# Kernel optimization log

Measured on AMD Instinct MI355X. Metric: run time of the kernel, lower is better.

The kernel has to match this reference:

```python
import jax, jax.numpy as jnp
import numpy as np

DIM = 2048
N_HEADS = 16
Q_LORA = 1536
KV_LORA = 512
NOPE = 128
ROPE = 64
V_DIM = 128
QK_HEAD = NOPE + ROPE
SEQ = 4096
THETA = 10000.0
EPS = 1e-6
SCALE = QK_HEAD ** -0.5  # max_seq_len==4096 not >4096, so no mscale adjustment


def rms_norm(x, w):
    return x * jax.lax.rsqrt(jnp.mean(x * x, axis=-1, keepdims=True) + EPS) * w


def rope_cos_sin(seqlen):
    inv_freq = 1.0 / THETA ** (jnp.arange(0, ROPE, 2, dtype=jnp.float32) / ROPE)  # [ROPE/2]
    t = jnp.arange(seqlen, dtype=jnp.float32)
    freqs = jnp.outer(t, inv_freq)  # [S, ROPE/2]
    return jnp.cos(freqs), jnp.sin(freqs)


def apply_rope(x, cos, sin):
    # x: (b, s, h, ROPE); pairs (x0, x1) rotated as complex mult, interleaved layout
    b, s, h, d = x.shape
    xr = x.reshape(b, s, h, d // 2, 2)
    x0, x1 = xr[..., 0], xr[..., 1]
    c = cos[None, :, None, :]
    sn = sin[None, :, None, :]
    out = jnp.stack([x0 * c - x1 * sn, x0 * sn + x1 * c], axis=-1)
    return out.reshape(b, s, h, d)


def setup_inputs() -> dict:
    key = jax.random.key(0)
    ks = jax.random.split(key, 8)
    s = lambda fan_in: 1.0 / np.sqrt(fan_in)
    return {
        "x": jax.random.normal(ks[0], (1, SEQ, DIM), jnp.float32),
        "wq_a_w": jax.random.normal(ks[1], (Q_LORA, DIM), jnp.float32) * s(DIM),
        "q_norm_w": 1.0 + 0.02 * jax.random.normal(ks[2], (Q_LORA,), jnp.float32),
        "wq_b_w": jax.random.normal(ks[3], (N_HEADS * QK_HEAD, Q_LORA), jnp.float32) * s(Q_LORA),
        "wkv_a_w": jax.random.normal(ks[4], (KV_LORA + ROPE, DIM), jnp.float32) * s(DIM),
        "kv_norm_w": 1.0 + 0.02 * jax.random.normal(ks[5], (KV_LORA,), jnp.float32),
        "wkv_b_w": jax.random.normal(ks[6], (N_HEADS * (NOPE + V_DIM), KV_LORA), jnp.float32) * s(KV_LORA),
        "wo_w": jax.random.normal(ks[7], (DIM, DIM), jnp.float32) * s(DIM),
    }


def reference(x, wq_a_w, q_norm_w, wq_b_w, wkv_a_w, kv_norm_w, wkv_b_w, wo_w):
    b, seqlen, _ = x.shape
    cos, sin = rope_cos_sin(seqlen)

    # Q path: low-rank down-proj -> RMSNorm -> up-proj
    q = rms_norm(x @ wq_a_w.T, q_norm_w) @ wq_b_w.T
    q = q.reshape(b, seqlen, N_HEADS, QK_HEAD)
    q_nope, q_pe = q[..., :NOPE], q[..., NOPE:]
    q_pe = apply_rope(q_pe, cos, sin)

    # KV path: compressed latent + decoupled rope key
    kv_a = x @ wkv_a_w.T  # (b, s, KV_LORA + ROPE)
    kv_latent, k_pe_raw = kv_a[..., :KV_LORA], kv_a[..., KV_LORA:]
    kv = rms_norm(kv_latent, kv_norm_w)               # (b, t, c)
    k_pe = apply_rope(k_pe_raw[:, :, None, :], cos, sin)[:, :, 0, :]  # (b, t, r)

    # Absorption trick: fold wkv_b's K-part into q_nope, attend against latents
    wkv_b = wkv_b_w.reshape(N_HEADS, NOPE + V_DIM, KV_LORA)
    q_abs = jnp.einsum("bshd,hdc->bshc", q_nope, wkv_b[:, :NOPE])

    scores = (jnp.einsum("bshc,btc->bsht", q_abs, kv)
              + jnp.einsum("bshr,btr->bsht", q_pe, k_pe)) * SCALE

    # causal additive mask over (s_query, t_key)
    causal = jnp.tril(jnp.ones((seqlen, seqlen), dtype=bool))
    scores = jnp.where(causal[None, :, None, :], scores, jnp.float32(-1e30))
    attn = jax.nn.softmax(scores, axis=-1)

    # post-softmax: aggregate latents, then recover V via wkv_b's V-part
    ctx = jnp.einsum("bsht,btc->bshc", attn, kv)
    v = jnp.einsum("bshc,hdc->bshd", ctx, wkv_b[:, NOPE:])  # (b, s, h, V_DIM)
    out = v.reshape(b, seqlen, N_HEADS * V_DIM) @ wo_w.T
    return out
```

## Files before the change

### kernel.cpp

```cpp
#include <hip/hip_runtime.h>

typedef unsigned short u16;
typedef __attribute__((ext_vector_type(8))) short bf16x8;
typedef __attribute__((ext_vector_type(4))) float f32x4;
typedef __attribute__((ext_vector_type(4))) unsigned short u16x4;

#define MFMA16(a, b, c) __builtin_amdgcn_mfma_f32_16x16x32_bf16((a), (b), (c), 0, 0, 0)

#define SEQ 4096
#define SCALE 0.07216878364870323f
#define LOGTHETA 9.210340371976184f

__device__ __forceinline__ u16 f2bf(float f) {
  union { float f; unsigned u; } c; c.f = f;
  unsigned u = c.u;
  unsigned r = (u + 0x7fffu + ((u >> 16) & 1u)) >> 16;
  return (u16)r;
}
__device__ __forceinline__ float bf2f(u16 b) {
  union { unsigned u; float f; } c; c.u = ((unsigned)b) << 16;
  return c.f;
}

__global__ void cvt_all(const float* __restrict__ x, const float* __restrict__ wqa,
                        const float* __restrict__ wqb, const float* __restrict__ wkva,
                        const float* __restrict__ wkvb, const float* __restrict__ wo,
                        u16* __restrict__ xb, u16* __restrict__ wqab,
                        u16* __restrict__ wqbb, u16* __restrict__ wkvab,
                        u16* __restrict__ wkvbb, u16* __restrict__ wob) {
  const int e0 = 2097152;
  const int e1 = e0 + 786432;
  const int e2 = e1 + 1179648;
  const int e3 = e2 + 294912;
  const int e4 = e3 + 524288;
  const int e5 = e4 + 1048576;
  int stride = gridDim.x * blockDim.x;
  for (int i = blockIdx.x * blockDim.x + threadIdx.x; i < e5; i += stride) {
    const float* src; u16* dst; int j;
    if (i < e0)      { src = x;    dst = xb;    j = i; }
    else if (i < e1) { src = wqa;  dst = wqab;  j = i - e0; }
    else if (i < e2) { src = wqb;  dst = wqbb;  j = i - e1; }
    else if (i < e3) { src = wkva; dst = wkvab; j = i - e2; }
    else if (i < e4) { src = wkvb; dst = wkvbb; j = i - e3; }
    else             { src = wo;   dst = wob;   j = i - e4; }
    f32x4 v = ((const f32x4*)src)[j];
    u16x4 o;
    o[0] = f2bf(v[0]); o[1] = f2bf(v[1]); o[2] = f2bf(v[2]); o[3] = f2bf(v[3]);
    ((u16x4*)dst)[j] = o;
  }
}

__global__ void trans_wkvb(const float* __restrict__ w, u16* __restrict__ wt) {
  int stride = gridDim.x * blockDim.x;
  for (int i = blockIdx.x * blockDim.x + threadIdx.x; i < 16 * 512 * 128; i += stride) {
    int h = i >> 16;
    int r = i & 65535;
    int c = r >> 7, d = r & 127;
    wt[i] = f2bf(w[(h * 256 + d) * 512 + c]);
  }
}

__global__ void trans_vt(const u16* __restrict__ cc, u16* __restrict__ vt2) {
  __shared__ u16 tile[64][65];
  int c0 = blockIdx.x * 64;
  int t0 = blockIdx.y * 64;
  for (int k = 0; k < 16; k++) {
    int el = threadIdx.x + k * 256;
    int r = el >> 6, c = el & 63;
    tile[r][c] = cc[(t0 + r) * 2112 + 1536 + c0 + c];
  }
  __syncthreads();
  for (int k = 0; k < 16; k++) {
    int el = threadIdx.x + k * 256;
    int r = el >> 6, c = el & 63;
    int t = t0 + c;
    vt2[(t >> 5) * 16384 + (c0 + r) * 32 + (t & 31)] = tile[c][r];
  }
}

__global__ void rms_q_kernel(u16* __restrict__ cc, const float* __restrict__ w) {
  int row = blockIdx.x;
  u16* p = cc + (size_t)row * 2112;
  float vals[6];
  float ss = 0.f;
#pragma unroll
  for (int k = 0; k < 6; k++) {
    float v = bf2f(p[threadIdx.x + k * 256]);
    vals[k] = v;
    ss += v * v;
  }
  for (int m = 1; m < 64; m <<= 1) ss += __shfl_xor(ss, m);
  __shared__ float red[4];
  int wid = threadIdx.x >> 6;
  if ((threadIdx.x & 63) == 0) red[wid] = ss;
  __syncthreads();
  float tot = red[0] + red[1] + red[2] + red[3];
  float rr = rsqrtf(tot / 1536.f + 1e-6f);
#pragma unroll
  for (int k = 0; k < 6; k++) {
    int i = threadIdx.x + k * 256;
    p[i] = f2bf(vals[k] * rr * w[i]);
  }
}

__global__ void rms_kv_kernel(u16* __restrict__ cc, const float* __restrict__ w) {
  int t = blockIdx.x;
  u16* p = cc + (size_t)t * 2112 + 1536;
  float v0 = bf2f(p[threadIdx.x]);
  float v1 = bf2f(p[threadIdx.x + 256]);
  float ss = v0 * v0 + v1 * v1;
  for (int m = 1; m < 64; m <<= 1) ss += __shfl_xor(ss, m);
  __shared__ float red[4];
  int wid = threadIdx.x >> 6;
  if ((threadIdx.x & 63) == 0) red[wid] = ss;
  __syncthreads();
  float tot = red[0] + red[1] + red[2] + red[3];
  float rr = rsqrtf(tot / 512.f + 1e-6f);
  p[threadIdx.x] = f2bf(v0 * rr * w[threadIdx.x]);
  p[threadIdx.x + 256] = f2bf(v1 * rr * w[threadIdx.x + 256]);
  if (threadIdx.x < 32) {
    int i = threadIdx.x;
    float x0 = bf2f(p[512 + 2 * i]);
    float x1 = bf2f(p[512 + 2 * i + 1]);
    float invf = expf(-((float)(2 * i) / 64.f) * LOGTHETA);
    float ang = (float)t * invf;
    float cs = cosf(ang), sn = sinf(ang);
    p[512 + 2 * i] = f2bf(x0 * cs - x1 * sn);
    p[512 + 2 * i + 1] = f2bf(x0 * sn + x1 * cs);
  }
}

__global__ void rope_q_kernel(const u16* __restrict__ qb, u16* __restrict__ qcat) {
  int stride = gridDim.x * blockDim.x;
  for (int idx = blockIdx.x * blockDim.x + threadIdx.x; idx < 4096 * 512; idx += stride) {
    int s = idx >> 9;
    int r = idx & 511;
    int h = r >> 5, i = r & 31;
    float x0 = bf2f(qb[s * 3072 + h * 192 + 128 + 2 * i]);
    float x1 = bf2f(qb[s * 3072 + h * 192 + 128 + 2 * i + 1]);
    float invf = expf(-((float)(2 * i) / 64.f) * LOGTHETA);
    float ang = (float)s * invf;
    float cs = cosf(ang) * SCALE, sn = sinf(ang) * SCALE;
    qcat[s * 9216 + h * 576 + 512 + 2 * i] = f2bf(x0 * cs - x1 * sn);
    qcat[s * 9216 + h * 576 + 512 + 2 * i + 1] = f2bf(x0 * sn + x1 * cs);
  }
}

template <int BN, bool OUTF32>
__launch_bounds__(256)
__global__ void gemm_tiled(const u16* __restrict__ A, int lda, int az,
                           const u16* __restrict__ W, int ldw, int wz,
                           void* __restrict__ Cp, int ldc, int cz, int K, float oscale,
                           int nvalid) {
  constexpr int NCH = 8 + BN / 16;
  constexpr int NBF = BN / 32;
  __shared__ __align__(16) u16 lds[2][NCH * 512];

  int z = blockIdx.z;
  int wid = threadIdx.x >> 6, lane = threadIdx.x & 63;
  int quad = lane >> 4, l16 = lane & 15;
  int wr = wid >> 1, wc = wid & 1;
  int m0 = blockIdx.y * 128;
  int n0 = blockIdx.x * BN;

  const u16* Az = A + (size_t)z * az;
  const u16* Wz = W + (size_t)z * wz;

  f32x4 acc[4][NBF];
#pragma unroll
  for (int i = 0; i < 4; i++)
#pragma unroll
    for (int j = 0; j < NBF; j++) acc[i][j] = {0.f, 0.f, 0.f, 0.f};

#pragma unroll
  for (int jj = 0; jj < NCH / 4; jj++) {
    int c = jj * 4 + wid;
    const u16* src = (c < 8) ? (Az + (m0 + c * 16 + l16) * (size_t)lda + quad * 8)
                             : (Wz + (n0 + (c - 8) * 16 + l16) * (size_t)ldw + quad * 8);
    __builtin_amdgcn_global_load_lds(
        (const __attribute__((address_space(1))) unsigned int*)src,
        (__attribute__((address_space(3))) unsigned int*)&lds[0][c * 512], 16, 0, 0);
  }

  int buf = 0;
  for (int k0 = 0; k0 < K; k0 += 32) {
    __syncthreads();
    if (k0 + 32 < K) {
      int k1 = k0 + 32;
#pragma unroll
      for (int jj = 0; jj < NCH / 4; jj++) {
        int c = jj * 4 + wid;
        const u16* src = (c < 8) ? (Az + (m0 + c * 16 + l16) * (size_t)lda + k1 + quad * 8)
                                 : (Wz + (n0 + (c - 8) * 16 + l16) * (size_t)ldw + k1 + quad * 8);
        __builtin_amdgcn_global_load_lds(
            (const __attribute__((address_space(1))) unsigned int*)src,
            (__attribute__((address_space(3))) unsigned int*)&lds[buf ^ 1][c * 512], 16, 0, 0);
      }
    }
    const u16* base = &lds[buf][0];
    bf16x8 a[4], b[NBF];
#pragma unroll
    for (int i = 0; i < 4; i++)
      a[i] = *(const bf16x8*)(base + (wr * 4 + i) * 512 + lane * 8);
#pragma unroll
    for (int j = 0; j < NBF; j++)
      b[j] = *(const bf16x8*)(base + (8 + wc * NBF + j) * 512 + lane * 8);
#pragma unroll
    for (int i = 0; i < 4; i++)
#pragma unroll
      for (int j = 0; j < NBF; j++) acc[i][j] = MFMA16(a[i], b[j], acc[i][j]);
    buf ^= 1;
  }

#pragma unroll
  for (int i = 0; i < 4; i++) {
    int row = m0 + wr * 64 + i * 16 + quad * 4;
#pragma unroll
    for (int j = 0; j < NBF; j++) {
      int col = n0 + wc * (BN / 2) + j * 16 + l16;
      if (col < nvalid) {
#pragma unroll
        for (int r = 0; r < 4; r++) {
          size_t cbase = (size_t)z * cz + (size_t)(row + r) * ldc + col;
          if (OUTF32) ((float*)Cp)[cbase] = acc[i][j][r] * oscale;
          else        ((u16*)Cp)[cbase] = f2bf(acc[i][j][r] * oscale);
        }
      }
    }
  }
}

__launch_bounds__(512, 2)
__global__ void attn_kernel(const u16* __restrict__ qcat, const u16* __restrict__ kcat,
                            const u16* __restrict__ vt2, u16* __restrict__ ctx) {
  __shared__ __align__(16) u16 lds[2][34816];
  __shared__ __align__(16) u16 plds[8][16][40];

  int wid = threadIdx.x >> 6, lane = threadIdx.x & 63;
  int quad = lane >> 4, l16 = lane & 15;
  int bx = blockIdx.x;
  int h = bx & 15;
  int jb = 31 - (bx >> 4);
  int qb0 = jb << 7;
  int m0 = qb0 + wid * 16;

  bf16x8 q[18];
  {
    const u16* qb = qcat + (m0 + l16) * 9216 + h * 576 + quad * 8;
#pragma unroll
    for (int kk = 0; kk < 18; kk++) q[kk] = *(const bf16x8*)(qb + kk * 32);
  }

  f32x4 zero = {0.f, 0.f, 0.f, 0.f};
  f32x4 o[32];
#pragma unroll
  for (int ct = 0; ct < 32; ct++) o[ct] = zero;
  float li[4] = {0.f, 0.f, 0.f, 0.f};

  int nt = (qb0 >> 5) + 4;

  const u16* sp[9];
  int sstr[9], soff[9];
  bool sact[9];
#pragma unroll
  for (int jj = 0; jj < 9; jj++) {
    int c = jj * 8 + wid;
    sact[jj] = (c < 68);
    soff[jj] = c * 512;
    if (c < 36) {
      int kk = c >> 1, half = c & 1;
      sp[jj] = kcat + (half * 16 + l16) * 2112 + kk * 32 + quad * 8;
      sstr[jj] = 32 * 2112;
    } else {
      int ct = c - 36;
      sp[jj] = vt2 + (ct * 16 + l16) * 32 + quad * 8;
      sstr[jj] = 16384;
    }
  }

#pragma unroll
  for (int jj = 0; jj < 9; jj++) {
    if (sact[jj]) {
      __builtin_amdgcn_global_load_lds(
          (const __attribute__((address_space(1))) unsigned int*)sp[jj],
          (__attribute__((address_space(3))) unsigned int*)&lds[0][soff[jj]], 16, 0, 0);
      sp[jj] += sstr[jj];
    }
  }

  for (int ti = 0; ti < nt; ti++) {
    __syncthreads();
    int buf = ti & 1;
    if (ti + 1 < nt) {
      u16* dbase = &lds[buf ^ 1][0];
#pragma unroll
      for (int jj = 0; jj < 9; jj++) {
        if (sact[jj]) {
          __builtin_amdgcn_global_load_lds(
              (const __attribute__((address_space(1))) unsigned int*)sp[jj],
              (__attribute__((address_space(3))) unsigned int*)&dbase[soff[jj]], 16, 0, 0);
          sp[jj] += sstr[jj];
        }
      }
    }

    int t0 = ti << 5;
    if (t0 <= m0 + 15) {
      const u16* kb = &lds[buf][0];
      const u16* vb = &lds[buf][18432];
      f32x4 s0 = zero, s1 = zero;
#pragma unroll
      for (int kk = 0; kk < 18; kk++) {
        bf16x8 b0 = *(const bf16x8*)(&kb[(kk * 2 + 0) * 512 + lane * 8]);
        bf16x8 b1 = *(const bf16x8*)(&kb[(kk * 2 + 1) * 512 + lane * 8]);
        s0 = MFMA16(q[kk], b0, s0);
        s1 = MFMA16(q[kk], b1, s1);
      }
      int tc0 = t0 + l16, tc1 = t0 + 16 + l16;
#pragma unroll
      for (int r = 0; r < 4; r++) {
        int mrow = m0 + quad * 4 + r;
        float e0 = (tc0 <= mrow) ? __expf(s0[r]) : 0.f;
        float e1 = (tc1 <= mrow) ? __expf(s1[r]) : 0.f;
        li[r] += e0 + e1;
        plds[wid][quad * 4 + r][l16] = f2bf(e0);
        plds[wid][quad * 4 + r][16 + l16] = f2bf(e1);
      }
      __threadfence_block();
      bf16x8 ap = *(const bf16x8*)(&plds[wid][l16][quad * 8]);
#pragma unroll
      for (int ct = 0; ct < 32; ct++) {
        bf16x8 bv = *(const bf16x8*)(&vb[ct * 512 + lane * 8]);
        o[ct] = MFMA16(ap, bv, o[ct]);
      }
    }
  }

#pragma unroll
  for (int r = 0; r < 4; r++) {
    float s = li[r];
    s += __shfl_xor(s, 1);
    s += __shfl_xor(s, 2);
    s += __shfl_xor(s, 4);
    s += __shfl_xor(s, 8);
    li[r] = s;
  }
  f32x4 inv = {1.f / li[0], 1.f / li[1], 1.f / li[2], 1.f / li[3]};
#pragma unroll
  for (int ct = 0; ct < 32; ct++) {
    f32x4 val = o[ct] * inv;
    int base = (m0 + quad * 4) * 8192 + h * 512 + ct * 16 + l16;
    ctx[base] = f2bf(val[0]);
    ctx[base + 8192] = f2bf(val[1]);
    ctx[base + 2 * 8192] = f2bf(val[2]);
    ctx[base + 3 * 8192] = f2bf(val[3]);
  }
}

extern "C" void kernel_launch(void* const* d_in, const int* in_sizes, int n_in,
                              void* d_out, int out_size, void* d_ws, size_t ws_size,
                              hipStream_t stream) {
  const float* x = (const float*)d_in[0];
  const float* wqa = (const float*)d_in[1];
  const float* qnw = (const float*)d_in[2];
  const float* wqb = (const float*)d_in[3];
  const float* wkva = (const float*)d_in[4];
  const float* kvnw = (const float*)d_in[5];
  const float* wkvb = (const float*)d_in[6];
  const float* wo = (const float*)d_in[7];

  u16* ws = (u16*)d_ws;
  u16* XB = ws;
  u16* WQAB = ws + 8388608;
  u16* WKVAB = ws + 11534336;
  u16* WQBB = ws + 12713984;
  u16* WKVBB = ws + 17432576;
  u16* WKVBT = ws + 19529728;
  u16* WOB = ws + 20578304;
  u16* CC = ws + 24772608;
  u16* VT = ws + 33423360;
  u16* QCAT = ws + 35520512;
  u16* CTX = ws + 73269248;
  u16* QB = CTX;
  u16* VBUF = QCAT;

  dim3 blk(256);

  cvt_all<<<2048, blk, 0, stream>>>(x, wqa, wqb, wkva, wkvb, wo,
                                    XB, WQAB, WQBB, WKVAB, WKVBB, WOB);
  trans_wkvb<<<1024, blk, 0, stream>>>(wkvb, WKVBT);

  gemm_tiled<128, false><<<dim3(17, 32, 1), blk, 0, stream>>>(
      XB, 2048, 0, WQAB, 2048, 0, CC, 2112, 0, 2048, 1.f, 2112);

  rms_q_kernel<<<4096, blk, 0, stream>>>(CC, qnw);
  rms_kv_kernel<<<4096, blk, 0, stream>>>(CC, kvnw);
  trans_vt<<<dim3(8, 64), blk, 0, stream>>>(CC, VT);

  gemm_tiled<128, false><<<dim3(24, 32, 1), blk, 0, stream>>>(
      CC, 2112, 0, WQBB, 1536, 0, QB, 3072, 0, 1536, 1.f, 1 << 30);

  gemm_tiled<128, false><<<dim3(4, 32, 16), blk, 0, stream>>>(
      QB, 3072, 192, WKVBT, 128, 65536, QCAT, 9216, 576, 128, SCALE, 1 << 30);
  rope_q_kernel<<<2048, blk, 0, stream>>>(QB, QCAT);

  attn_kernel<<<512, dim3(512), 0, stream>>>(QCAT, CC + 1536, VT, CTX);

  gemm_tiled<128, false><<<dim3(1, 32, 16), blk, 0, stream>>>(
      CTX, 8192, 512, WKVBB + 65536, 512, 131072, VBUF, 2048, 128, 512, 1.f, 1 << 30);

  gemm_tiled<128, true><<<dim3(16, 32, 1), blk, 0, stream>>>(
      VBUF, 2048, 0, WOB, 2048, 0, d_out, 2048, 0, 2048, 1.f, 1 << 30);
}
```

Measured before the change: 902.5 us.

## Add 256x256-tile GEMM kernel for large projection matmuls

Introduces a 512-thread GEMM with 256x256 output tiles and double-buffered direct-to-LDS loads, and uses it for the Q/KV down-projection, Q up-projection and output projection. Larger tiles raise data reuse per loaded byte and cut global traffic. In exchange the grids shrink to fewer blocks than there are CUs, and the large LDS footprint limits occupancy, which may leave the GPU underutilised.

```diff
diff --git a/kernel.cpp b/kernel.cpp
--- a/kernel.cpp
+++ b/kernel.cpp
@@ -146,6 +146,106 @@
   }
 }
 
+template <bool OUTF32>
+__launch_bounds__(512, 2)
+__global__ void gemm256(const u16* __restrict__ A, int lda,
+                        const u16* __restrict__ W, int ldw,
+                        void* __restrict__ Cp, int ldc, int K, float oscale,
+                        int nvalid) {
+  __shared__ __align__(16) u16 lds[2][32768];
+
+  int wid = threadIdx.x >> 6, lane = threadIdx.x & 63;
+  int quad = lane >> 4, l16 = lane & 15;
+  int wr = wid >> 2, wc = wid & 3;
+  int m0 = blockIdx.y * 256;
+  int n0 = blockIdx.x * 256;
+
+  f32x4 acc[8][4];
+#pragma unroll
+  for (int i = 0; i < 8; i++)
+#pragma unroll
+    for (int j = 0; j < 4; j++) acc[i][j] = {0.f, 0.f, 0.f, 0.f};
+
+  const u16* sp[8];
+  int soff[8];
+#pragma unroll
+  for (int jj = 0; jj < 8; jj++) {
+    int c = jj * 8 + wid;
+    soff[jj] = c * 512 + lane * 8;
+    if (c < 32) {
+      int rb = c >> 1, kh = c & 1;
+      sp[jj] = A + (size_t)(m0 + rb * 16 + l16) * lda + kh * 32 + quad * 8;
+    } else {
+      int cb = c - 32, nb = cb >> 1, kh = cb & 1;
+      int row = n0 + nb * 16 + l16;
+      if (row >= nvalid) row = nvalid - 1;
+      sp[jj] = W + (size_t)row * ldw + kh * 32 + quad * 8;
+    }
+  }
+
+  int nkt = K >> 6;
+
+#pragma unroll
+  for (int jj = 0; jj < 8; jj++) {
+    __builtin_amdgcn_global_load_lds(
+        (const __attribute__((address_space(1))) unsigned int*)sp[jj],
+        (__attribute__((address_space(3))) unsigned int*)&lds[0][soff[jj]], 16, 0, 0);
+    sp[jj] += 64;
+  }
+  asm volatile("s_waitcnt vmcnt(0)" ::: "memory");
+  __builtin_amdgcn_s_barrier();
+  __builtin_amdgcn_sched_barrier(0);
+
+  int buf = 0;
+  for (int kt = 0; kt < nkt; kt++) {
+    if (kt + 1 < nkt) {
+#pragma unroll
+      for (int jj = 0; jj < 8; jj++) {
+        __builtin_amdgcn_global_load_lds(
+            (const __attribute__((address_space(1))) unsigned int*)sp[jj],
+            (__attribute__((address_space(3))) unsigned int*)&lds[buf ^ 1][soff[jj]], 16, 0, 0);
+        sp[jj] += 64;
+      }
+    }
+    const u16* base = &lds[buf][0];
+#pragma unroll
+    for (int kh = 0; kh < 2; kh++) {
+      bf16x8 a[8], b[4];
+#pragma unroll
+      for (int i = 0; i < 8; i++)
+        a[i] = *(const bf16x8*)(base + ((wr * 8 + i) * 2 + kh) * 512 + lane * 8);
+#pragma unroll
+      for (int j = 0; j < 4; j++)
+        b[j] = *(const bf16x8*)(base + (32 + (wc * 4 + j) * 2 + kh) * 512 + lane * 8);
+#pragma unroll
+      for (int i = 0; i < 8; i++)
+#pragma unroll
+        for (int j = 0; j < 4; j++) acc[i][j] = MFMA16(a[i], b[j], acc[i][j]);
+    }
+    asm volatile("s_waitcnt vmcnt(0)" ::: "memory");
+    __builtin_amdgcn_s_barrier();
+    __builtin_amdgcn_sched_barrier(0);
+    buf ^= 1;
+  }
+
+#pragma unroll
+  for (int i = 0; i < 8; i++) {
+    int row = m0 + wr * 128 + i * 16 + quad * 4;
+#pragma unroll
+    for (int j = 0; j < 4; j++) {
+      int col = n0 + wc * 64 + j * 16 + l16;
+      if (col < nvalid) {
+#pragma unroll
+        for (int r = 0; r < 4; r++) {
+          size_t cbase = (size_t)(row + r) * ldc + col;
+          if (OUTF32) ((float*)Cp)[cbase] = acc[i][j][r] * oscale;
+          else        ((u16*)Cp)[cbase] = f2bf(acc[i][j][r] * oscale);
+        }
+      }
+    }
+  }
+}
+
 template <int BN, bool OUTF32>
 __launch_bounds__(256)
 __global__ void gemm_tiled(const u16* __restrict__ A, int lda, int az,
@@ -390,15 +490,15 @@
                                     XB, WQAB, WQBB, WKVAB, WKVBB, WOB);
   trans_wkvb<<<1024, blk, 0, stream>>>(wkvb, WKVBT);
 
-  gemm_tiled<128, false><<<dim3(17, 32, 1), blk, 0, stream>>>(
-      XB, 2048, 0, WQAB, 2048, 0, CC, 2112, 0, 2048, 1.f, 2112);
+  gemm256<false><<<dim3(9, 16), dim3(512), 0, stream>>>(
+      XB, 2048, WQAB, 2048, CC, 2112, 2048, 1.f, 2112);
 
   rms_q_kernel<<<4096, blk, 0, stream>>>(CC, qnw);
   rms_kv_kernel<<<4096, blk, 0, stream>>>(CC, kvnw);
   trans_vt<<<dim3(8, 64), blk, 0, stream>>>(CC, VT);
 
-  gemm_tiled<128, false><<<dim3(24, 32, 1), blk, 0, stream>>>(
-      CC, 2112, 0, WQBB, 1536, 0, QB, 3072, 0, 1536, 1.f, 1 << 30);
+  gemm256<false><<<dim3(12, 16), dim3(512), 0, stream>>>(
+      CC, 2112, WQBB, 1536, QB, 3072, 1536, 1.f, 3072);
 
   gemm_tiled<128, false><<<dim3(4, 32, 16), blk, 0, stream>>>(
       QB, 3072, 192, WKVBT, 128, 65536, QCAT, 9216, 576, 128, SCALE, 1 << 30);
@@ -409,6 +509,6 @@
   gemm_tiled<128, false><<<dim3(1, 32, 16), blk, 0, stream>>>(
       CTX, 8192, 512, WKVBB + 65536, 512, 131072, VBUF, 2048, 128, 512, 1.f, 1 << 30);
 
-  gemm_tiled<128, true><<<dim3(16, 32, 1), blk, 0, stream>>>(
-      VBUF, 2048, 0, WOB, 2048, 0, d_out, 2048, 0, 2048, 1.f, 1 << 30);
-}
+  gemm256<true><<<dim3(8, 16), dim3(512), 0, stream>>>(
+      VBUF, 2048, WOB, 2048, d_out, 2048, 2048, 1.f, 2048);
+}
```

New measurement: 909.2 us. Within noise of the previous version (+0.7%).
